# Kernel optimization log

Hardware: AMD Instinct MI355X
Metric: run time of the kernel (lower is better)

## Reference

```python
import jax, jax.numpy as jnp
import numpy as np

V, B, T, R, U, L, S = 8000, 64, 256, 1024, 512, 3, 1024


def setup_inputs() -> dict:
    key = jax.random.key(0)
    ks = jax.random.split(key, 12)
    sd = 0.05
    stdv = float(np.sqrt(1.0 / V))
    return {
        "input_data": jax.random.randint(ks[0], (B, T), 0, V, dtype=jnp.int32),
        "targets": jax.random.randint(ks[1], (B, T), 0, V, dtype=jnp.int32),
        "sampled": jax.random.randint(ks[2], (S,), 0, V, dtype=jnp.int32),
        "true_expected_counts": jax.random.uniform(ks[3], (B * T,), minval=0.01, maxval=1.0),
        "sampled_expected_counts": jax.random.uniform(ks[4], (S,), minval=0.01, maxval=1.0),
        "embedding": jax.random.uniform(ks[5], (V, U), minval=-stdv, maxval=stdv),
        "Wh0": jax.random.normal(ks[6], (U + R, R)) * sd,
        "bh0": jnp.zeros((R,)),
        "Wt0": jax.random.normal(ks[7], (U + R, R)) * sd,
        "bt0": -jnp.ones((R,)),  # bias_start = -1.0 for transform gate
        "Wh": jax.random.normal(ks[8], (L - 1, R, R)) * sd,
        "bh": jnp.zeros((L - 1, R)),
        "Wt": jax.random.normal(ks[9], (L - 1, R, R)) * sd,
        "bt": -jnp.ones((L - 1, R)),
        "Wp": jax.random.normal(ks[10], (R, U)) * sd,
        "bp": jnp.zeros((U,)),
        "softmax_w": jax.random.normal(ks[11], (V, U)) * sd,
        "softmax_b": jnp.zeros((V,)),
    }


def reference(input_data, targets, sampled, true_expected_counts,
              sampled_expected_counts, embedding, Wh0, bh0, Wt0, bt0,
              Wh, bh, Wt, bt, Wp, bp, softmax_w, softmax_b):
    # embedding lookup (keep_prob=1.0 -> input dropout is a no-op)
    x = embedding[input_data]              # [B,T,U]
    xs = jnp.transpose(x, (1, 0, 2))       # [T,B,U] for time-major scan

    def step(state, xt):
        # highway layer 0: sees [input, state]
        cat = jnp.concatenate([xt, state], axis=1)       # [B,U+R]
        h = jnp.tanh(cat @ Wh0 + bh0)
        t = jax.nn.sigmoid(cat @ Wt0 + bt0)
        state = (h - state) * t + state
        # highway layers 1..L-1: state only
        for l in range(L - 1):
            h = jnp.tanh(state @ Wh[l] + bh[l])
            t = jax.nn.sigmoid(state @ Wt[l] + bt[l])
            state = (h - state) * t + state
        return state, state

    state0 = jnp.zeros((B, R), dtype=x.dtype)
    final_state, states = jax.lax.scan(step, state0, xs)   # states: [T,B,R]

    # OutputProjectionWrapper: per-step linear rnn_size -> num_units
    outputs = states @ Wp + bp                              # [T,B,U]
    outputs = jnp.transpose(outputs, (1, 0, 2)).reshape(B * T, U)

    # sampled softmax loss (fixed candidates, remove accidental hits)
    labels = targets.reshape(-1)                            # [N]
    w_true = softmax_w[labels]                              # [N,U]
    b_true = softmax_b[labels]                              # [N]
    true_logits = jnp.sum(outputs * w_true, axis=-1) + b_true \
        - jnp.log(true_expected_counts)                     # [N]
    sampled_logits = outputs @ softmax_w[sampled].T + softmax_b[sampled] \
        - jnp.log(sampled_expected_counts)                  # [N,S]
    acc_hit = labels[:, None] == sampled[None, :]
    sampled_logits = jnp.where(acc_hit, sampled_logits - 1e9, sampled_logits)

    logits = jnp.concatenate([true_logits[:, None], sampled_logits], axis=1)
    loss = -jax.nn.log_softmax(logits, axis=1)[:, 0]        # true class at idx 0
    cost = jnp.mean(loss)
    return cost
```

## Files before the change

kernel.cpp:

```cpp
#include <hip/hip_runtime.h>
#include <hip/hip_bf16.h>
#include <hip/hip_fp16.h>

#define Vv 8000
#define Bb 64
#define Tt 256
#define Rr 1024
#define Uu 512
#define Ll 3
#define Sn 1024
#define Nrows (Bb*Tt)
#define NWG2 256
#define CNTSTRIDE 1024

typedef __attribute__((ext_vector_type(8))) short short8;
typedef __attribute__((ext_vector_type(4))) float f32x4;
typedef __attribute__((ext_vector_type(4))) unsigned int u32x4;
typedef unsigned long long u64t;

static __device__ inline f32x4 mfma16(short8 a, short8 b, f32x4 c) {
    return __builtin_amdgcn_mfma_f32_16x16x32_bf16(a, b, c, 0, 0, 0);
}

static __device__ inline float bf2f(unsigned short u) {
    union { unsigned int i; float f; } v; v.i = ((unsigned int)u) << 16; return v.f;
}
static __device__ inline unsigned short f2bf(float f) {
    union { float f; unsigned int i; } v; v.f = f;
    unsigned int x = v.i;
    unsigned int r = (x + 0x7fffu + ((x >> 16) & 1u)) >> 16;
    return (unsigned short)r;
}
static __device__ inline unsigned short f2h(float f) {
    __half h = __float2half(f);
    union { __half h; unsigned short u; } v; v.h = h; return v.u;
}
static __device__ inline float h2f(unsigned short u) {
    union { unsigned short u; __half h; } v; v.u = u; return __half2float(v.h);
}

#if __has_builtin(__builtin_amdgcn_rcpf)
#define RCPF(x) __builtin_amdgcn_rcpf(x)
#else
#define RCPF(x) (1.0f/(x))
#endif

static __device__ __forceinline__ void ldg16_coh(u32x4* d, u64t a) {
    asm volatile("global_load_dwordx4 %0, %1, off sc0 sc1" : "=v"(*d) : "v"(a));
}
static __device__ __forceinline__ void st2_coh(u64t a, unsigned short v) {
    asm volatile("global_store_short %0, %1, off sc0 sc1" :: "v"(a), "v"((unsigned)v) : "memory");
}
static __device__ __forceinline__ unsigned ld_flag_coh(const unsigned int* p) {
    unsigned v;
    asm volatile("global_load_dword %0, %1, off sc0 sc1\n\ts_waitcnt vmcnt(0)"
                 : "=v"(v) : "v"((u64t)p) : "memory");
    return v;
}

__global__ __launch_bounds__(256) void detect_kernel(const unsigned short* __restrict__ tec,
                                                     int* __restrict__ flag) {
    __shared__ int cnt;
    if (threadIdx.x == 0) cnt = 0;
    __syncthreads();
    float f = bf2f(tec[threadIdx.x]);
    int ok = (f >= 0.0078125f && f <= 1.0f) ? 1 : 0;
    atomicAdd(&cnt, ok);
    __syncthreads();
    if (threadIdx.x == 0) *flag = (cnt >= 240) ? 0 : 1;
}

__global__ __launch_bounds__(256) void cvt_kernel(const void* __restrict__ src,
                                                  unsigned short* __restrict__ dst,
                                                  int n, const int* __restrict__ flag) {
    int i = blockIdx.x * 256 + threadIdx.x;
    if (i >= n) return;
    if (*flag)
        dst[i] = f2bf(((const float*)src)[i]);
    else
        dst[i] = ((const unsigned short*)src)[i];
}

__global__ __launch_bounds__(256) void pack_direct(const unsigned short* __restrict__ W,
                                                   short* __restrict__ dst,
                                                   int KT, int NT, int N) {
    int tid = blockIdx.x * 256 + threadIdx.x;
    int total = KT * NT * 64;
    if (tid >= total) return;
    int lane = tid & 63;
    int tile = tid >> 6;
    int nt = tile % NT;
    int kt = tile / NT;
    int k0 = kt * 32 + (lane >> 4) * 8;
    int n  = nt * 16 + (lane & 15);
    short8 v;
#pragma unroll
    for (int j = 0; j < 8; ++j)
        v[j] = (short)W[(size_t)(k0 + j) * N + n];
    ((short8*)dst)[tid] = v;
}

__global__ __launch_bounds__(256) void pack_gather(const void* __restrict__ sw,
                                                   const int* __restrict__ sampled,
                                                   short* __restrict__ dst,
                                                   const int* __restrict__ flag) {
    int tid = blockIdx.x * 256 + threadIdx.x;
    int total = 16 * 64 * 64;
    if (tid >= total) return;
    int lane = tid & 63;
    int tile = tid >> 6;
    int nt = tile % 64;
    int kt = tile / 64;
    int k0 = kt * 32 + (lane >> 4) * 8;
    int n  = nt * 16 + (lane & 15);
    int row = sampled[n];
    short8 v;
    if (*flag) {
        const float* swf = (const float*)sw;
#pragma unroll
        for (int j = 0; j < 8; ++j)
            v[j] = (short)f2bf(swf[(size_t)row * Uu + k0 + j]);
    } else {
        const unsigned short* swu = (const unsigned short*)sw;
#pragma unroll
        for (int j = 0; j < 8; ++j)
            v[j] = (short)swu[(size_t)row * Uu + k0 + j];
    }
    ((short8*)dst)[tid] = v;
}

static __device__ __forceinline__ void slice_arrive(unsigned int* cnt) {
    __syncthreads();
    if (threadIdx.x == 0)
        __hip_atomic_fetch_add(cnt, 1u, __ATOMIC_RELAXED, __HIP_MEMORY_SCOPE_AGENT);
}
static __device__ __forceinline__ void slice_wait_wd(unsigned int* cnt, unsigned int tgt,
                                                     int* gaveup) {
    if (threadIdx.x == 0) {
        if (ld_flag_coh(cnt) < tgt) {
            unsigned long long t0 = __builtin_amdgcn_s_memrealtime();
            for (;;) {
                __builtin_amdgcn_s_sleep(4);
                if (ld_flag_coh(cnt) >= tgt) break;
                if (__builtin_amdgcn_s_memrealtime() - t0 > (1ull << 24)) {
                    *gaveup = 1;
                    break;
                }
            }
        }
    }
    __syncthreads();
}


#define LADDER_STEP(J, VM)                                                    \
    asm volatile("s_waitcnt vmcnt(" #VM ")" ::: "memory");                    \
    __builtin_amdgcn_sched_barrier(0);                                        \
    {                                                                         \
        short8 a1 = *(short8*)&ah[J];                                         \
        short8 a2 = *(short8*)&al[J];                                         \
        short8 bH, bT;                                                        \
        if (l == 0) { bH = whs[J]; bT = wts[J]; }                             \
        else {                                                                \
            int base = (l - 1) * 64;                                          \
            bH = WL[(base + (w * 8 + (J))) * 64 + lane];                      \
            bT = WL[(base + 32 + (w * 8 + (J))) * 64 + lane];                 \
        }                                                                     \
        if ((J) & 1) {                                                        \
            aH1 = mfma16(a1, bH, aH1); aH1 = mfma16(a2, bH, aH1);             \
            aT1 = mfma16(a1, bT, aT1); aT1 = mfma16(a2, bT, aT1);             \
        } else {                                                              \
            aH0 = mfma16(a1, bH, aH0); aH0 = mfma16(a2, bH, aH0);             \
            aT0 = mfma16(a1, bT, aT0); aT0 = mfma16(a2, bT, aT0);             \
        }                                                                     \
    }

__global__ __launch_bounds__(256, 1) void scan_kernel(
    const short8* __restrict__ pWh0, const short8* __restrict__ pWt0,
    const short8* __restrict__ pWh1, const short8* __restrict__ pWt1,
    const short8* __restrict__ pWh2, const short8* __restrict__ pWt2,
    const unsigned short* __restrict__ cbh0, const unsigned short* __restrict__ cbt0,
    const unsigned short* __restrict__ cbh,  const unsigned short* __restrict__ cbt,
    const unsigned short* __restrict__ embb, const int* __restrict__ tokens,
    unsigned short* __restrict__ stbuf, unsigned short* __restrict__ hist,
    unsigned int* cnt)
{
    __shared__ short8 WL[128 * 64];
    __shared__ float red[2048];
    __shared__ int gaveup;

    int tid  = threadIdx.x;
    int lane = tid & 63, w = tid >> 6;
    int quad = lane >> 4, l15 = lane & 15;
    int r = blockIdx.x & 3;
    int c = blockIdx.x >> 2;

    if (tid == 0) gaveup = 0;

#pragma unroll
    for (int i = 0; i < 32; ++i) {
        int e = i * 256 + tid;
        int tile = e >> 6;
        int ln = e & 63;
        int l12 = tile >> 6;
        int ht  = (tile >> 5) & 1;
        int kt  = tile & 31;
        const short8* src = l12 ? (ht ? pWt2 : pWh2) : (ht ? pWt1 : pWh1);
        WL[e] = src[((size_t)kt * 64 + c) * 64 + ln];
    }
    short8 whe[4], wte[4], whs[8], wts[8];
#pragma unroll
    for (int j = 0; j < 4; ++j) {
        whe[j] = pWh0[((size_t)(4 * w + j) * 64 + c) * 64 + lane];
        wte[j] = pWt0[((size_t)(4 * w + j) * 64 + c) * 64 + lane];
    }
#pragma unroll
    for (int j = 0; j < 8; ++j) {
        whs[j] = pWh0[((size_t)(16 + 8 * w + j) * 64 + c) * 64 + lane];
        wts[j] = pWt0[((size_t)(16 + 8 * w + j) * 64 + c) * 64 + lane];
    }
    __syncthreads();

    int crow = tid >> 4, ccol = tid & 15;
    int colg = 16 * c + ccol;
    float bh0v = bf2f(cbh0[colg]), bh1v = bf2f(cbh[colg]), bh2v = bf2f(cbh[1024 + colg]);
    float bt0v = bf2f(cbt0[colg]), bt1v = bf2f(cbt[colg]), bt2v = bf2f(cbt[1024 + colg]);
    size_t so = (size_t)(r * 16 + crow) * 1024 + colg;
    float s_old = 0.f;

    int rowA = r * 16 + l15;
    unsigned int* mycnt = cnt + r * CNTSTRIDE;
    unsigned short* hi0 = stbuf;
    unsigned short* lo0 = stbuf + 65536;
    unsigned short* hi1 = stbuf + 131072;
    unsigned short* lo1 = stbuf + 196608;

    f32x4 eH = {0,0,0,0}, eT = {0,0,0,0};
    {
        int token = tokens[rowA * Tt];
#pragma unroll
        for (int j = 0; j < 4; ++j) {
            short8 ae = *(const short8*)(embb + (size_t)token * Uu
                                         + w * 128 + j * 32 + quad * 8);
            eH = mfma16(ae, whe[j], eH);
            eT = mfma16(ae, wte[j], eT);
        }
    }

    int l = 0, t = 0;
    int dead = 0;
    for (int i = 0; i < 768; ++i) {
        if (i && !dead) {
            slice_wait_wd(mycnt, 64u * (unsigned)i, &gaveup);
            dead = gaveup;
        }

        const unsigned short* hsrc = (l == 0 && i) ? hist + (size_t)(t - 1) * 65536
                                                   : ((i & 1) ? hi1 : hi0);
        const unsigned short* lsrc = (i & 1) ? lo1 : lo0;
        u32x4 ah[8], al[8];
        size_t abase = (size_t)rowA * 1024 + w * 256 + quad * 8;
#pragma unroll
        for (int j = 0; j < 8; ++j) {
            ldg16_coh(&ah[j], (u64t)(hsrc + abase + j * 32));
            ldg16_coh(&al[j], (u64t)(lsrc + abase + j * 32));
        }

        f32x4 aH0, aH1, aT0, aT1;
        if (l == 0) { aH0 = eH; aT0 = eT; }
        else        { aH0 = (f32x4){0,0,0,0}; aT0 = (f32x4){0,0,0,0}; }
        aH1 = (f32x4){0,0,0,0}; aT1 = (f32x4){0,0,0,0};
        LADDER_STEP(0, 14)
        LADDER_STEP(1, 12)
        LADDER_STEP(2, 10)
        LADDER_STEP(3, 8)
        LADDER_STEP(4, 6)
        LADDER_STEP(5, 4)
        LADDER_STEP(6, 2)
        LADDER_STEP(7, 0)

#pragma unroll
        for (int ri = 0; ri < 4; ++ri) {
            int cell = (quad * 4 + ri) * 16 + l15;
            red[(w * 2 + 0) * 256 + cell] = aH0[ri] + aH1[ri];
            red[(w * 2 + 1) * 256 + cell] = aT0[ri] + aT1[ri];
        }
        __syncthreads();
        float Hs = red[tid] + red[512 + tid] + red[1024 + tid] + red[1536 + tid];
        float Ts = red[256 + tid] + red[768 + tid] + red[1280 + tid] + red[1792 + tid];

        float bhl = (l == 0) ? bh0v : ((l == 1) ? bh1v : bh2v);
        float btl = (l == 0) ? bt0v : ((l == 1) ? bt1v : bt2v);
        float xh = Hs + bhl;
        float ehx = __expf(xh + xh);
        float hh = 1.0f - 2.0f * RCPF(ehx + 1.0f);
        float xt = Ts + btl;
        float gg = RCPF(1.0f + __expf(-xt));
        float sn = (hh - s_old) * gg + s_old;
        s_old = sn;
        unsigned short hb = f2bf(sn);
        unsigned short lb = f2bf(sn - bf2f(hb));
        unsigned short* hdst = (l == 2) ? hist + (size_t)t * 65536
                                        : (((i + 1) & 1) ? hi1 : hi0);
        unsigned short* ldst = ((i + 1) & 1) ? lo1 : lo0;
        st2_coh((u64t)(hdst + so), hb);
        st2_coh((u64t)(ldst + so), lb);

        slice_arrive(mycnt);

        if (l == 2) {
            int tn = (t + 1 < Tt) ? t + 1 : t;
            int token = tokens[rowA * Tt + tn];
            eH = (f32x4){0,0,0,0}; eT = (f32x4){0,0,0,0};
#pragma unroll
            for (int j = 0; j < 4; ++j) {
                short8 ae = *(const short8*)(embb + (size_t)token * Uu
                                             + w * 128 + j * 32 + quad * 8);
                eH = mfma16(ae, whe[j], eH);
                eT = mfma16(ae, wte[j], eT);
            }
            l = 0; ++t;
        } else {
            ++l;
        }
    }
}

__global__ __launch_bounds__(256) void proj_kernel(
    const unsigned short* __restrict__ hist, const short8* __restrict__ pB,
    const unsigned short* __restrict__ bp, unsigned short* __restrict__ proj)
{
    int lane = threadIdx.x & 63, wave = threadIdx.x >> 6;
    int quad = lane >> 4, l15 = lane & 15;
    int m0 = blockIdx.x * 64 + wave * 16;
    int n0 = blockIdx.y * 64;
    f32x4 acc[4];
#pragma unroll
    for (int c = 0; c < 4; ++c) acc[c] = (f32x4){0.f, 0.f, 0.f, 0.f};

    const unsigned short* arow = hist + (size_t)(m0 + l15) * Rr;
    for (int kt = 0; kt < 32; ++kt) {
        short8 a = *(const short8*)(arow + kt * 32 + quad * 8);
#pragma unroll
        for (int c = 0; c < 4; ++c) {
            short8 b = pB[((size_t)kt * 32 + (n0 >> 4) + c) * 64 + lane];
            acc[c] = mfma16(a, b, acc[c]);
        }
    }
#pragma unroll
    for (int c = 0; c < 4; ++c) {
        int col = n0 + c * 16 + l15;
        float bpv = bf2f(bp[col]);
#pragma unroll
        for (int r = 0; r < 4; ++r) {
            int row = m0 + quad * 4 + r;
            proj[(size_t)row * Uu + col] = f2bf(acc[c][r] + bpv);
        }
    }
}

__global__ __launch_bounds__(256) void sampled_kernel(
    const unsigned short* __restrict__ proj, const short8* __restrict__ pB,
    const unsigned short* __restrict__ sb, const int* __restrict__ sampled,
    const int* __restrict__ targets, const unsigned short* __restrict__ sec,
    unsigned short* __restrict__ slog)
{
    int lane = threadIdx.x & 63, wave = threadIdx.x >> 6;
    int quad = lane >> 4, l15 = lane & 15;
    int m0 = blockIdx.x * 64 + wave * 16;
    int n0 = blockIdx.y * 64;
    f32x4 acc[4];
#pragma unroll
    for (int c = 0; c < 4; ++c) acc[c] = (f32x4){0.f, 0.f, 0.f, 0.f};

    const unsigned short* arow = proj + (size_t)(m0 + l15) * Uu;
    for (int kt = 0; kt < 16; ++kt) {
        short8 a = *(const short8*)(arow + kt * 32 + quad * 8);
#pragma unroll
        for (int c = 0; c < 4; ++c) {
            short8 b = pB[((size_t)kt * 64 + (n0 >> 4) + c) * 64 + lane];
            acc[c] = mfma16(a, b, acc[c]);
        }
    }
#pragma unroll
    for (int c = 0; c < 4; ++c) {
        int j = n0 + c * 16 + l15;
        int sj = sampled[j];
        float bias = bf2f(sb[sj]) - logf(bf2f(sec[j]));
#pragma unroll
        for (int r = 0; r < 4; ++r) {
            int row = m0 + quad * 4 + r;
            int n_idx = ((row & 63) << 8) + (row >> 6);
            int label = targets[n_idx];
            float lg = acc[c][r] + bias;
            if (label == sj) lg = -30000.0f;
            slog[(size_t)row * Sn + j] = f2h(lg);
        }
    }
}

__global__ __launch_bounds__(256) void true_kernel(
    const unsigned short* __restrict__ proj, const void* __restrict__ sw,
    const unsigned short* __restrict__ sb, const int* __restrict__ targets,
    const unsigned short* __restrict__ tec, float* __restrict__ tl,
    const int* __restrict__ flagp)
{
    int lane = threadIdx.x & 63;
    int m = blockIdx.x * 4 + (threadIdx.x >> 6);
    int n_idx = ((m & 63) << 8) + (m >> 6);
    int label = targets[n_idx];
    short8 a = *(const short8*)(proj + (size_t)m * Uu + lane * 8);
    float s = 0.f;
    if (*flagp) {
        const float* bw = (const float*)sw + (size_t)label * Uu + lane * 8;
        float4 b0 = *(const float4*)bw;
        float4 b1 = *(const float4*)(bw + 4);
        float bb[8] = {b0.x, b0.y, b0.z, b0.w, b1.x, b1.y, b1.z, b1.w};
#pragma unroll
        for (int j = 0; j < 8; ++j)
            s += bf2f((unsigned short)a[j]) * bb[j];
    } else {
        short8 b = *(const short8*)((const unsigned short*)sw + (size_t)label * Uu + lane * 8);
#pragma unroll
        for (int j = 0; j < 8; ++j)
            s += bf2f((unsigned short)a[j]) * bf2f((unsigned short)b[j]);
    }
#pragma unroll
    for (int mask = 32; mask >= 1; mask >>= 1) s += __shfl_xor(s, mask);
    if (lane == 0)
        tl[m] = s + bf2f(sb[label]) - logf(bf2f(tec[n_idx]));
}

__global__ __launch_bounds__(256) void lse_kernel(
    const unsigned short* __restrict__ slog, const float* __restrict__ tl,
    float* __restrict__ loss_sum)
{
    int lane = threadIdx.x & 63;
    int m = blockIdx.x * 4 + (threadIdx.x >> 6);
    const short8* p = (const short8*)(slog + (size_t)m * Sn);
    short8 v0 = p[lane * 2];
    short8 v1 = p[lane * 2 + 1];
    float v[16];
#pragma unroll
    for (int j = 0; j < 8; ++j) { v[j] = h2f((unsigned short)v0[j]); v[8 + j] = h2f((unsigned short)v1[j]); }
    float mx = v[0];
#pragma unroll
    for (int j = 1; j < 16; ++j) mx = fmaxf(mx, v[j]);
#pragma unroll
    for (int mask = 32; mask >= 1; mask >>= 1) mx = fmaxf(mx, __shfl_xor(mx, mask));
    float se = 0.f;
#pragma unroll
    for (int j = 0; j < 16; ++j) se += expf(v[j] - mx);
#pragma unroll
    for (int mask = 32; mask >= 1; mask >>= 1) se += __shfl_xor(se, mask);
    if (lane == 0) {
        float tlv = tl[m];
        float mm  = fmaxf(mx, tlv);
        float tot = se * expf(mx - mm) + expf(tlv - mm);
        atomicAdd(loss_sum, mm + logf(tot) - tlv);
    }
}

__global__ void fin_kernel(const float* __restrict__ loss_sum, unsigned int* __restrict__ out) {
    float v = loss_sum[0] * (1.0f / (float)Nrows);
    unsigned int H = (unsigned int)f2bf(v);
    out[0] = (H << 16) | H;
}

extern "C" void kernel_launch(void* const* d_in, const int* in_sizes, int n_in,
                              void* d_out, int out_size, void* d_ws, size_t ws_size,
                              hipStream_t stream) {
    (void)in_sizes; (void)n_in; (void)out_size; (void)ws_size;

    const int*  input_data = (const int*)d_in[0];
    const int*  targets    = (const int*)d_in[1];
    const int*  sampled    = (const int*)d_in[2];
    const void* tec        = d_in[3];
    const void* sec        = d_in[4];
    const void* emb        = d_in[5];
    const void* Wh0        = d_in[6];
    const void* bh0        = d_in[7];
    const void* Wt0        = d_in[8];
    const void* bt0        = d_in[9];
    const void* Wh         = d_in[10];
    const void* bh         = d_in[11];
    const void* Wt         = d_in[12];
    const void* bt         = d_in[13];
    const void* Wp         = d_in[14];
    const void* bp         = d_in[15];
    const void* sw         = d_in[16];
    const void* sb         = d_in[17];

    char* ws = (char*)d_ws;
    size_t off = 0;
    short* pWh0 = (short*)(ws + off); off += (size_t)48 * 64 * 512 * 2;
    short* pWt0 = (short*)(ws + off); off += (size_t)48 * 64 * 512 * 2;
    short* pWh1 = (short*)(ws + off); off += (size_t)32 * 64 * 512 * 2;
    short* pWh2 = (short*)(ws + off); off += (size_t)32 * 64 * 512 * 2;
    short* pWt1 = (short*)(ws + off); off += (size_t)32 * 64 * 512 * 2;
    short* pWt2 = (short*)(ws + off); off += (size_t)32 * 64 * 512 * 2;
    short* pWp  = (short*)(ws + off); off += (size_t)32 * 32 * 512 * 2;
    short* pSW  = (short*)(ws + off); off += (size_t)16 * 64 * 512 * 2;
    unsigned short* cbh0 = (unsigned short*)(ws + off); off += 1024 * 2;
    unsigned short* cbt0 = (unsigned short*)(ws + off); off += 1024 * 2;
    unsigned short* cbh  = (unsigned short*)(ws + off); off += 2048 * 2;
    unsigned short* cbt  = (unsigned short*)(ws + off); off += 2048 * 2;
    unsigned short* cbp  = (unsigned short*)(ws + off); off += 512 * 2;
    unsigned short* csb  = (unsigned short*)(ws + off); off += 8000 * 2;
    unsigned short* ctec = (unsigned short*)(ws + off); off += 16384 * 2;
    unsigned short* csec = (unsigned short*)(ws + off); off += 1024 * 2;
    unsigned short* stbuf = (unsigned short*)(ws + off); off += (size_t)4 * 65536 * 2;
    unsigned short* hist = (unsigned short*)(ws + off); off += (size_t)Nrows * Rr * 2;
    unsigned short* proj = (unsigned short*)(ws + off); off += (size_t)Nrows * Uu * 2;
    unsigned short* slog = (unsigned short*)(ws + off); off += (size_t)Nrows * Sn * 2;
    float* tl   = (float*)(ws + off); off += (size_t)Nrows * 4;
    float* loss = (float*)(ws + off); off += 256;
    int*   flag = (int*)(ws + off);   off += 256;
    off = (off + 4095) & ~(size_t)4095;
    unsigned int* barrier_mem = (unsigned int*)(ws + off); off += 8 * 4096;

    unsigned int* cnt = barrier_mem;

    unsigned short* cWh0 = (unsigned short*)slog;
    unsigned short* cWt0 = cWh0 + (size_t)1536 * 1024;
    unsigned short* cWh  = cWt0 + (size_t)1536 * 1024;
    unsigned short* cWt  = cWh  + (size_t)2 * 1024 * 1024;
    unsigned short* cWp  = cWt  + (size_t)2 * 1024 * 1024;
    unsigned short* embb = (unsigned short*)proj;

    hipMemsetAsync(stbuf, 0, (size_t)2 * 65536 * 2, stream);
    hipMemsetAsync(loss, 0, 4, stream);
    hipMemsetAsync(barrier_mem, 0, 8 * 4096, stream);

    detect_kernel<<<1, 256, 0, stream>>>((const unsigned short*)tec, flag);
#define CVT(src, dst, n) cvt_kernel<<<((n) + 255) / 256, 256, 0, stream>>>(src, dst, n, flag)
    CVT(bh0, cbh0, 1024);
    CVT(bt0, cbt0, 1024);
    CVT(bh,  cbh,  2048);
    CVT(bt,  cbt,  2048);
    CVT(bp,  cbp,  512);
    CVT(sb,  csb,  8000);
    CVT(tec, ctec, 16384);
    CVT(sec, csec, 1024);
    CVT(emb, embb, 8000 * 512);
    CVT(Wh0, cWh0, 1536 * 1024);
    CVT(Wt0, cWt0, 1536 * 1024);
    CVT(Wh,  cWh,  2 * 1024 * 1024);
    CVT(Wt,  cWt,  2 * 1024 * 1024);
    CVT(Wp,  cWp,  1024 * 512);
#undef CVT

    pack_direct<<<(48 * 64 * 64 + 255) / 256, 256, 0, stream>>>(cWh0, pWh0, 48, 64, 1024);
    pack_direct<<<(48 * 64 * 64 + 255) / 256, 256, 0, stream>>>(cWt0, pWt0, 48, 64, 1024);
    pack_direct<<<(32 * 64 * 64 + 255) / 256, 256, 0, stream>>>(cWh,               pWh1, 32, 64, 1024);
    pack_direct<<<(32 * 64 * 64 + 255) / 256, 256, 0, stream>>>(cWh + 1024 * 1024, pWh2, 32, 64, 1024);
    pack_direct<<<(32 * 64 * 64 + 255) / 256, 256, 0, stream>>>(cWt,               pWt1, 32, 64, 1024);
    pack_direct<<<(32 * 64 * 64 + 255) / 256, 256, 0, stream>>>(cWt + 1024 * 1024, pWt2, 32, 64, 1024);
    pack_direct<<<(32 * 32 * 64 + 255) / 256, 256, 0, stream>>>(cWp, pWp, 32, 32, 512);
    pack_gather<<<(16 * 64 * 64 + 255) / 256, 256, 0, stream>>>(sw, sampled, pSW, flag);

    scan_kernel<<<NWG2, 256, 0, stream>>>(
        (const short8*)pWh0, (const short8*)pWt0,
        (const short8*)pWh1, (const short8*)pWt1,
        (const short8*)pWh2, (const short8*)pWt2,
        cbh0, cbt0, cbh, cbt,
        embb, input_data,
        stbuf, hist, cnt);

    proj_kernel<<<dim3(256, 8), 256, 0, stream>>>(hist, (const short8*)pWp, cbp, proj);
    true_kernel<<<Nrows / 4, 256, 0, stream>>>(proj, sw, csb, targets, ctec, tl, flag);
    sampled_kernel<<<dim3(256, 16), 256, 0, stream>>>(proj, (const short8*)pSW, csb,
                                                      sampled, targets, csec, slog);
    lse_kernel<<<Nrows / 4, 256, 0, stream>>>(slog, tl, loss);
    fin_kernel<<<1, 1, 0, stream>>>(loss, (unsigned int*)d_out);
}
```

Before: 3.450 ms.

## Replace atomic counter barrier with per-workgroup flags polled in parallel

The per-slice barrier in the persistent scan kernel no longer has all 64 workgroups atomically increment one shared counter. Each workgroup now stores its step number into its own flag word, and 64 threads each poll one flag, with a shorter sleep between polls. This removes atomic contention and serialisation on a single cache line at each of the 768 sequential steps. The LDS reduction buffer indexing is also XOR-swizzled to cut bank conflicts. In exchange, every step does 64 polling loads per workgroup instead of one.

Result: no change. 3.466 ms (+0.5%).

```diff
diff --git a/kernel.cpp b/kernel.cpp
--- a/kernel.cpp
+++ b/kernel.cpp
@@ -11,7 +11,6 @@
 #define Sn 1024
 #define Nrows (Bb*Tt)
 #define NWG2 256
-#define CNTSTRIDE 1024
 
 typedef __attribute__((ext_vector_type(8))) short short8;
 typedef __attribute__((ext_vector_type(4))) float f32x4;
@@ -50,6 +49,9 @@
 }
 static __device__ __forceinline__ void st2_coh(u64t a, unsigned short v) {
     asm volatile("global_store_short %0, %1, off sc0 sc1" :: "v"(a), "v"((unsigned)v) : "memory");
+}
+static __device__ __forceinline__ void st4_coh(u64t a, unsigned v) {
+    asm volatile("global_store_dword %0, %1, off sc0 sc1" :: "v"(a), "v"(v) : "memory");
 }
 static __device__ __forceinline__ unsigned ld_flag_coh(const unsigned int* p) {
     unsigned v;
@@ -129,19 +131,20 @@
     ((short8*)dst)[tid] = v;
 }
 
-static __device__ __forceinline__ void slice_arrive(unsigned int* cnt) {
+static __device__ __forceinline__ void flag_arrive(unsigned int* fl, unsigned val) {
     __syncthreads();
     if (threadIdx.x == 0)
-        __hip_atomic_fetch_add(cnt, 1u, __ATOMIC_RELAXED, __HIP_MEMORY_SCOPE_AGENT);
-}
-static __device__ __forceinline__ void slice_wait_wd(unsigned int* cnt, unsigned int tgt,
-                                                     int* gaveup) {
-    if (threadIdx.x == 0) {
-        if (ld_flag_coh(cnt) < tgt) {
+        st4_coh((u64t)fl, val);
+}
+static __device__ __forceinline__ void flag_wait_wd(const unsigned int* flags, unsigned tgt,
+                                                    int* gaveup) {
+    if (threadIdx.x < 64) {
+        const unsigned int* fp = flags + threadIdx.x;
+        if (ld_flag_coh(fp) < tgt) {
             unsigned long long t0 = __builtin_amdgcn_s_memrealtime();
             for (;;) {
-                __builtin_amdgcn_s_sleep(4);
-                if (ld_flag_coh(cnt) >= tgt) break;
+                __builtin_amdgcn_s_sleep(2);
+                if (ld_flag_coh(fp) >= tgt) break;
                 if (__builtin_amdgcn_s_memrealtime() - t0 > (1ull << 24)) {
                     *gaveup = 1;
                     break;
@@ -183,7 +186,7 @@
     const unsigned short* __restrict__ cbh,  const unsigned short* __restrict__ cbt,
     const unsigned short* __restrict__ embb, const int* __restrict__ tokens,
     unsigned short* __restrict__ stbuf, unsigned short* __restrict__ hist,
-    unsigned int* cnt)
+    unsigned int* fb)
 {
     __shared__ short8 WL[128 * 64];
     __shared__ float red[2048];
@@ -227,9 +230,11 @@
     float bt0v = bf2f(cbt0[colg]), bt1v = bf2f(cbt[colg]), bt2v = bf2f(cbt[1024 + colg]);
     size_t so = (size_t)(r * 16 + crow) * 1024 + colg;
     float s_old = 0.f;
+    int rsw = tid ^ ((tid >> 6) & 3);
 
     int rowA = r * 16 + l15;
-    unsigned int* mycnt = cnt + r * CNTSTRIDE;
+    unsigned int* myflags = fb + r * 1024;
+    unsigned int* myflag  = myflags + c;
     unsigned short* hi0 = stbuf;
     unsigned short* lo0 = stbuf + 65536;
     unsigned short* hi1 = stbuf + 131072;
@@ -251,7 +256,7 @@
     int dead = 0;
     for (int i = 0; i < 768; ++i) {
         if (i && !dead) {
-            slice_wait_wd(mycnt, 64u * (unsigned)i, &gaveup);
+            flag_wait_wd(myflags, (unsigned)i, &gaveup);
             dead = gaveup;
         }
 
@@ -281,13 +286,13 @@
 
 #pragma unroll
         for (int ri = 0; ri < 4; ++ri) {
-            int cell = (quad * 4 + ri) * 16 + l15;
+            int cell = ((quad * 4 + ri) * 16 + l15) ^ quad;
             red[(w * 2 + 0) * 256 + cell] = aH0[ri] + aH1[ri];
             red[(w * 2 + 1) * 256 + cell] = aT0[ri] + aT1[ri];
         }
         __syncthreads();
-        float Hs = red[tid] + red[512 + tid] + red[1024 + tid] + red[1536 + tid];
-        float Ts = red[256 + tid] + red[768 + tid] + red[1280 + tid] + red[1792 + tid];
+        float Hs = red[rsw] + red[512 + rsw] + red[1024 + rsw] + red[1536 + rsw];
+        float Ts = red[256 + rsw] + red[768 + rsw] + red[1280 + rsw] + red[1792 + rsw];
 
         float bhl = (l == 0) ? bh0v : ((l == 1) ? bh1v : bh2v);
         float btl = (l == 0) ? bt0v : ((l == 1) ? bt1v : bt2v);
@@ -306,7 +311,7 @@
         st2_coh((u64t)(hdst + so), hb);
         st2_coh((u64t)(ldst + so), lb);
 
-        slice_arrive(mycnt);
+        flag_arrive(myflag, (unsigned)(i + 1));
 
         if (l == 2) {
             int tn = (t + 1 < Tt) ? t + 1 : t;
@@ -519,7 +524,7 @@
     off = (off + 4095) & ~(size_t)4095;
     unsigned int* barrier_mem = (unsigned int*)(ws + off); off += 8 * 4096;
 
-    unsigned int* cnt = barrier_mem;
+    unsigned int* fb = barrier_mem;
 
     unsigned short* cWh0 = (unsigned short*)slog;
     unsigned short* cWt0 = cWh0 + (size_t)1536 * 1024;
@@ -565,7 +570,7 @@
         (const short8*)pWh2, (const short8*)pWt2,
         cbh0, cbt0, cbh, cbt,
         embb, input_data,
-        stbuf, hist, cnt);
+        stbuf, hist, fb);
 
     proj_kernel<<<dim3(256, 8), 256, 0, stream>>>(hist, (const short8*)pWp, cbp, proj);
     true_kernel<<<Nrows / 4, 256, 0, stream>>>(proj, sw, csb, targets, ctec, tl, flag);
```
